# Kernel optimization log

Measured on AMD Instinct MI355X. Metric: run time of the kernel, lower is better.

Reference implementation:

```python
import jax, jax.numpy as jnp
import numpy as np
from jax import lax

B, T, U, H, V = 4, 256, 48, 512, 1024
BLANK = V - 1  # blank = vocab_size - 1, as in Transducer.__init__


def setup_inputs() -> dict:
    key = jax.random.key(0)
    k1, k2, k3, k4 = jax.random.split(key, 4)
    enc_state = jax.random.normal(k1, (B, T, H), jnp.float32)       # encoder output
    dec_state = jax.random.normal(k2, (B, U + 1, H), jnp.float32)   # decoder output (blank-prepended targets)
    W = jax.random.normal(k3, (V, H), jnp.float32) / np.sqrt(H)     # joint proj weight
    b = jnp.zeros((V,), jnp.float32)                                # joint proj bias
    targets = jax.random.randint(k4, (B, U), 0, V - 1).astype(jnp.int32)  # labels, never blank
    inputs_length = jnp.full((B,), T, jnp.int32)
    targets_length = jnp.full((B,), U, jnp.int32)
    return {"enc_state": enc_state, "dec_state": dec_state, "W": W, "b": b,
            "targets": targets, "inputs_length": inputs_length,
            "targets_length": targets_length}


def _rnnt_loss_single(log_probs, targets, t_len, u_len):
    # log_probs: (T, U+1, V); forward-variable alpha DP of RNNT loss.
    lp_blank = log_probs[:, :, BLANK]                                   # (T, U+1)
    lp_label = jnp.take_along_axis(log_probs[:, :-1, :],
                                   targets[None, :, None], axis=2)[..., 0]  # (T, U)
    # first row: only label emissions, alpha[0,u] = sum_{k<u} lp_label[0,k]
    row0 = jnp.concatenate([jnp.zeros((1,), log_probs.dtype),
                            jnp.cumsum(lp_label[0])])                   # (U+1,)

    def row_step(prev_row, t):
        # alpha[t,u] = logaddexp(alpha[t-1,u] + blank[t-1,u], alpha[t,u-1] + label[t,u-1])
        a = prev_row + lp_blank[t - 1]                                  # (U+1,) blank transitions

        def u_step(carry, xs):
            a_u, lab = xs
            cur = jnp.logaddexp(a_u, carry + lab)
            return cur, cur

        _, rest = lax.scan(u_step, a[0], (a[1:], lp_label[t]))
        row = jnp.concatenate([a[:1], rest])
        return row, row

    _, rows = lax.scan(row_step, row0, jnp.arange(1, T))
    alpha = jnp.concatenate([row0[None], rows], axis=0)                 # (T, U+1)
    # negative log-likelihood: final blank emission from (t_len-1, u_len)
    return -(alpha[t_len - 1, u_len] + lp_blank[t_len - 1, u_len])


def reference(enc_state, dec_state, W, b, targets, inputs_length, targets_length):
    # JointNet: broadcast-add (repeat in torch) then linear projection
    joint = enc_state[:, :, None, :] + dec_state[:, None, :, :]         # (B, T, U+1, H)
    logits = jnp.einsum('btuh,vh->btuv', joint, W) + b                  # (B, T, U+1, V)
    log_probs = jax.nn.log_softmax(logits, axis=-1)
    loss = jax.vmap(_rnnt_loss_single)(log_probs, targets, inputs_length, targets_length)
    return loss  # per-sample losses (reduction='None')
```

## Files before the change

### kernel.cpp

```cpp
#include <hip/hip_runtime.h>
#include <math.h>

#define B_ 4
#define T_ 256
#define U_ 48
#define H_ 512
#define V_ 1024
#define BLANK_ (V_-1)

#define GM 1220
#define GM_ENC 1024
#define APAD 1280

#define INVLN2 1.4426950408889634f
#define LN2F   0.6931471805599453f

typedef __attribute__((ext_vector_type(8))) short short8;
typedef __attribute__((ext_vector_type(4))) float f32x4;

__device__ __forceinline__ unsigned short f2bf(float x) {
    union { float f; unsigned int u; } c; c.f = x;
    unsigned int r = c.u + 0x7FFF + ((c.u >> 16) & 1);
    return (unsigned short)(r >> 16);
}
__device__ __forceinline__ float bf2f(unsigned short u) {
    union { unsigned int i; float f; } c; c.i = ((unsigned int)u) << 16; return c.f;
}
__device__ __forceinline__ unsigned int cvt_pk_bf16(float lo, float hi) {
    unsigned int r;
    asm("v_cvt_pk_bf16_f32 %0, %1, %2" : "=v"(r) : "v"(lo), "v"(hi));
    return r;
}
__device__ __forceinline__ int wave_shr1_i(int x, int fill) {
    return __builtin_amdgcn_update_dpp(fill, x, 0x138 , 0xf, 0xf, false);
}
__device__ __forceinline__ float wave_shr1_f(float x, float fill) {
    return __builtin_bit_cast(float,
        wave_shr1_i(__builtin_bit_cast(int, x), __builtin_bit_cast(int, fill)));
}

__global__ __launch_bounds__(256) void gemm1_kernel(
    const float* __restrict__ enc, const float* __restrict__ dec,
    const float* __restrict__ W, const float* __restrict__ bias,
    unsigned short* __restrict__ Pexp)
{
    __shared__ __attribute__((aligned(16))) unsigned short As[64 * 64];
    __shared__ __attribute__((aligned(16))) unsigned short Bs[64 * 64];
    const int tid  = threadIdx.x;
    const int lane = tid & 63, wave = tid >> 6;
    const int wm = wave >> 1, wn = wave & 1;
    const int row0 = blockIdx.y * 64, col0 = blockIdx.x * 64;
    const int srow = tid >> 2;
    const int scg  = (tid & 3) * 16;

    f32x4 acc[2][2];
    #pragma unroll
    for (int mi = 0; mi < 2; ++mi)
        #pragma unroll
        for (int ni = 0; ni < 2; ++ni)
            acc[mi][ni] = (f32x4){0.f, 0.f, 0.f, 0.f};

    const int gr = row0 + srow;
    const float* srcA = (gr < GM_ENC) ? enc + (size_t)gr * H_
                      : (gr < GM)     ? dec + (size_t)(gr - GM_ENC) * H_
                                      : (const float*)0;
    const float* srcB = W + (size_t)(col0 + srow) * H_;

    float4 ra[4], rb[4];
    auto loadAB = [&](int k0) {
        float4 z = make_float4(0.f, 0.f, 0.f, 0.f);
        ra[0] = ra[1] = ra[2] = ra[3] = z;
        if (srcA) {
            const float* s = srcA + k0 + scg;
            ra[0] = *(const float4*)s;       ra[1] = *(const float4*)(s + 4);
            ra[2] = *(const float4*)(s + 8); ra[3] = *(const float4*)(s + 12);
        }
        const float* s = srcB + k0 + scg;
        rb[0] = *(const float4*)s;       rb[1] = *(const float4*)(s + 4);
        rb[2] = *(const float4*)(s + 8); rb[3] = *(const float4*)(s + 12);
    };
    auto stage = [&]() {
        uint4 w0 = { cvt_pk_bf16(ra[0].x, ra[0].y), cvt_pk_bf16(ra[0].z, ra[0].w),
                     cvt_pk_bf16(ra[1].x, ra[1].y), cvt_pk_bf16(ra[1].z, ra[1].w) };
        uint4 w1 = { cvt_pk_bf16(ra[2].x, ra[2].y), cvt_pk_bf16(ra[2].z, ra[2].w),
                     cvt_pk_bf16(ra[3].x, ra[3].y), cvt_pk_bf16(ra[3].z, ra[3].w) };
        uint4 v0 = { cvt_pk_bf16(rb[0].x, rb[0].y), cvt_pk_bf16(rb[0].z, rb[0].w),
                     cvt_pk_bf16(rb[1].x, rb[1].y), cvt_pk_bf16(rb[1].z, rb[1].w) };
        uint4 v1 = { cvt_pk_bf16(rb[2].x, rb[2].y), cvt_pk_bf16(rb[2].z, rb[2].w),
                     cvt_pk_bf16(rb[3].x, rb[3].y), cvt_pk_bf16(rb[3].z, rb[3].w) };
        int colb = scg * 2;
        int sw0 = (colb)      ^ ((srow & 7) << 4);
        int sw1 = (colb + 16) ^ ((srow & 7) << 4);
        *(uint4*)((char*)As + srow * 128 + sw0) = w0;
        *(uint4*)((char*)As + srow * 128 + sw1) = w1;
        *(uint4*)((char*)Bs + srow * 128 + sw0) = v0;
        *(uint4*)((char*)Bs + srow * 128 + sw1) = v1;
    };
    auto compute = [&]() {
        #pragma unroll
        for (int kk = 0; kk < 2; ++kk) {
            short8 a[2], b[2];
            const int cb = kk * 64 + (lane >> 4) * 16;
            #pragma unroll
            for (int mi = 0; mi < 2; ++mi) {
                int r = wm * 32 + mi * 16 + (lane & 15);
                a[mi] = *(const short8*)((const char*)As + r * 128 + (cb ^ ((r & 7) << 4)));
            }
            #pragma unroll
            for (int ni = 0; ni < 2; ++ni) {
                int r = wn * 32 + ni * 16 + (lane & 15);
                b[ni] = *(const short8*)((const char*)Bs + r * 128 + (cb ^ ((r & 7) << 4)));
            }
            #pragma unroll
            for (int mi = 0; mi < 2; ++mi)
                #pragma unroll
                for (int ni = 0; ni < 2; ++ni)
                    asm("v_mfma_f32_16x16x32_bf16 %0, %1, %2, %0"
                        : "+v"(acc[mi][ni]) : "v"(a[mi]), "v"(b[ni]));
        }
    };

    loadAB(0);
    for (int k0 = 0; k0 < H_; k0 += 64) {
        stage();
        asm volatile("s_waitcnt lgkmcnt(0)" ::: "memory");
        __builtin_amdgcn_s_barrier();
        asm volatile("" ::: "memory");
        if (k0 + 64 < H_) loadAB(k0 + 64);
        compute();
        asm volatile("" ::: "memory");
        __builtin_amdgcn_s_barrier();
        asm volatile("" ::: "memory");
    }

    #pragma unroll
    for (int ni = 0; ni < 2; ++ni) {
        int col = col0 + wn * 32 + ni * 16 + (lane & 15);
        float bb = bias[col];
        #pragma unroll
        for (int mi = 0; mi < 2; ++mi) {
            #pragma unroll
            for (int j = 0; j < 4; ++j) {
                int r = row0 + wm * 32 + mi * 16 + (lane >> 4) * 4 + j;
                if (r >= GM) continue;
                float v = acc[mi][ni][j] + (r < GM_ENC ? bb : 0.f);
                Pexp[(size_t)r * V_ + col] = f2bf(__builtin_amdgcn_exp2f(v * INVLN2));
            }
        }
    }
}

__global__ __launch_bounds__(256) void gemm2_kernel(
    const unsigned short* __restrict__ Pexp, const int* __restrict__ targets,
    float* __restrict__ lp)
{
    __shared__ __attribute__((aligned(16))) unsigned short As[64 * 64];
    __shared__ __attribute__((aligned(16))) unsigned short Bs[64 * 64];
    __shared__ float eb[64];
    __shared__ float db[64];
    __shared__ float dg[64];
    __shared__ int   tgts[64];
    const int tid  = threadIdx.x;
    const int lane = tid & 63, wave = tid >> 6;
    const int wm = wave >> 1, wn = wave & 1;
    const int mt = blockIdx.x, b = blockIdx.y;

    if (tid < 64) {
        eb[tid] = bf2f(Pexp[(size_t)(b * 256 + mt * 64 + tid) * V_ + BLANK_]);
    } else if (tid < 128) {
        int u = tid - 64;
        if (u <= U_) {
            size_t drow = (size_t)(GM_ENC + b * (U_ + 1) + u);
            db[u] = bf2f(Pexp[drow * V_ + BLANK_]);
            if (u < U_) {
                int tg = targets[b * U_ + u];
                tgts[u] = tg;
                dg[u] = bf2f(Pexp[drow * V_ + tg]);
            }
        }
    }

    f32x4 acc[2][2];
    #pragma unroll
    for (int mi = 0; mi < 2; ++mi)
        #pragma unroll
        for (int ni = 0; ni < 2; ++ni)
            acc[mi][ni] = (f32x4){0.f, 0.f, 0.f, 0.f};

    short8 a2[2], b2[2];
    auto loadT = [&](int k0) {
        #pragma unroll
        for (int c = 0; c < 2; ++c) {
            int off = (tid + 256 * c) * 16;
            int row = off >> 7, colb = off & 127;
            size_t arow = (size_t)(b * 256 + mt * 64 + row);
            a2[c] = *(const short8*)((const char*)Pexp + arow * (V_*2) + k0*2 + colb);
            size_t brow = (size_t)(GM_ENC + b * (U_ + 1) + (row <= U_ ? row : U_));
            b2[c] = *(const short8*)((const char*)Pexp + brow * (V_*2) + k0*2 + colb);
        }
    };
    auto stageT = [&]() {
        #pragma unroll
        for (int c = 0; c < 2; ++c) {
            int off = (tid + 256 * c) * 16;
            int row = off >> 7, colb = off & 127;
            int sw = colb ^ ((row & 7) << 4);
            *(short8*)((char*)As + row * 128 + sw) = a2[c];
            *(short8*)((char*)Bs + row * 128 + sw) = b2[c];
        }
    };

    loadT(0);
    for (int k0 = 0; k0 < V_; k0 += 64) {
        stageT();
        asm volatile("s_waitcnt lgkmcnt(0)" ::: "memory");
        __builtin_amdgcn_s_barrier();
        asm volatile("" ::: "memory");
        if (k0 + 64 < V_) loadT(k0 + 64);
        #pragma unroll
        for (int kk = 0; kk < 2; ++kk) {
            short8 a[2], bfr[2];
            const int cb = kk * 64 + (lane >> 4) * 16;
            #pragma unroll
            for (int mi = 0; mi < 2; ++mi) {
                int r = wm * 32 + mi * 16 + (lane & 15);
                a[mi] = *(const short8*)((const char*)As + r * 128 + (cb ^ ((r & 7) << 4)));
            }
            #pragma unroll
            for (int ni = 0; ni < 2; ++ni) {
                int r = wn * 32 + ni * 16 + (lane & 15);
                bfr[ni] = *(const short8*)((const char*)Bs + r * 128 + (cb ^ ((r & 7) << 4)));
            }
            #pragma unroll
            for (int mi = 0; mi < 2; ++mi)
                #pragma unroll
                for (int ni = 0; ni < 2; ++ni)
                    asm("v_mfma_f32_16x16x32_bf16 %0, %1, %2, %0"
                        : "+v"(acc[mi][ni]) : "v"(a[mi]), "v"(bfr[ni]));
        }
        asm volatile("" ::: "memory");
        __builtin_amdgcn_s_barrier();
        asm volatile("" ::: "memory");
    }

    #pragma unroll
    for (int ni = 0; ni < 2; ++ni) {
        int u = wn * 32 + ni * 16 + (lane & 15);
        if (u > U_) continue;
        float dbu = db[u];
        float dgu = (u < U_) ? dg[u] : 0.f;
        int   tgu = (u < U_) ? tgts[u] : 0;
        #pragma unroll
        for (int mi = 0; mi < 2; ++mi) {
            #pragma unroll
            for (int j = 0; j < 4; ++j) {
                int tp = wm * 32 + mi * 16 + (lane >> 4) * 4 + j;
                int t  = mt * 64 + tp;
                float rd = __builtin_amdgcn_rcpf(acc[mi][ni][j]);
                lp[((size_t)b * 97 + u) * T_ + t] = eb[tp] * dbu * rd;
                if (u < U_) {
                    float eg = bf2f(Pexp[(size_t)(b * 256 + t) * V_ + tgu]);
                    lp[((size_t)b * 97 + 49 + u) * T_ + t] = eg * dgu * rd;
                }
            }
        }
    }
}

__global__ __launch_bounds__(256) void dp_kernel(
    const float* __restrict__ lp,
    const int* __restrict__ tlen, const int* __restrict__ ulen,
    float* __restrict__ out)
{
    __shared__ __attribute__((aligned(16))) float sm[97 * 257 + 3];
    const int b = blockIdx.x;
    const int tid = threadIdx.x;
    {
        const float4* g = (const float4*)(lp + (size_t)b * 97 * T_);
        for (int i = tid; i < 97 * T_ / 4; i += 256) {
            float4 v = g[i];
            int r = i >> 6;
            int t = (i & 63) << 2;
            float* d = sm + r * 257 + t;
            d[0] = v.x; d[1] = v.y; d[2] = v.z; d[3] = v.w;
        }
    }
    __syncthreads();
    if (tid >= 64) return;

    const int l = tid;
    const int TL = tlen[b], UL = ulen[b];
    const int lt = (TL - 1) >> 2;
    const int smax = lt + UL;

    const int ROWB = 257 * 4;
    const int bLo = 16 * l, bHi = 48 * ROWB + 16 * l;
    const int lLo = 49 * ROWB + 16 * l, lHi = 96 * ROWB + 16 * l;
    int wb = -l * ROWB + 16 * l;

    float M0 = 0.f, M1 = 0.f, M2 = 0.f, M3 = 0.f;
    int E = 0;
    float wprev = 0.f;

    struct Pay { float b0, b1, b2, b3, l0, l1, l2, l3; };
    Pay pA, pB;
    auto issue = [&](Pay& P) {
        int ab = min(max(wb, bLo), bHi);
        int al = min(max(wb + 48 * ROWB, lLo), lHi);
        const char* base = (const char*)sm;
        P.b0 = *(const float*)(base + ab);
        P.b1 = *(const float*)(base + ab + 4);
        P.b2 = *(const float*)(base + ab + 8);
        P.b3 = *(const float*)(base + ab + 12);
        P.l0 = *(const float*)(base + al);
        P.l1 = *(const float*)(base + al + 4);
        P.l2 = *(const float*)(base + al + 8);
        P.l3 = *(const float*)(base + al + 12);
        wb += ROWB;
    };
    auto step = [&](int s, const Pay& P) {
        float bm  = wave_shr1_f(M3, 0.f);
        int   bE  = wave_shr1_i(E, -(1 << 24));
        float B0f = wave_shr1_f(wprev, 0.f);
        wprev = P.b3;
        int u = s - l;
        if (u >= 0 && u <= U_) {
            bool act  = (u == 0);
            bool seed = (s == 0);
            int Eu = act ? bE : max(E, bE);
            if (seed) Eu = 0;
            float sb = ldexpf(bm, bE - Eu);
            float sO = act ? 0.f : ldexpf(1.0f, E - Eu);
            float m0 = M0 * sO, m1 = M1 * sO, m2 = M2 * sO, m3 = M3 * sO;
            float A0 = fmaf(sb, B0f, m0 * P.l0);
            if (seed) A0 = 1.0f;
            float A1 = fmaf(A0, P.b0, m1 * P.l1);
            float A2 = fmaf(A1, P.b1, m2 * P.l2);
            float A3 = fmaf(A2, P.b2, m3 * P.l3);
            float mx = fmaxf(fmaxf(A0, A1), fmaxf(A2, A3));
            int e = (int)((__builtin_bit_cast(unsigned, mx) >> 23) & 0xFF) - 126;
            M0 = ldexpf(A0, -e); M1 = ldexpf(A1, -e);
            M2 = ldexpf(A2, -e); M3 = ldexpf(A3, -e);
            E = Eu + e;
        }
    };

    issue(pA);
    issue(pB);
    int s = 0;
    for (; s + 1 <= smax; s += 2) {
        step(s, pA);     issue(pA);
        step(s + 1, pB); issue(pB);
    }
    if (s <= smax) step(s, pA);

    if (l == lt) {
        int j = (TL - 1) & 3;
        float rm = (j == 0) ? M0 : (j == 1) ? M1 : (j == 2) ? M2 : M3;
        float lfin = __builtin_amdgcn_logf(rm) + (float)E
                   + __builtin_amdgcn_logf(sm[UL * 257 + (TL - 1)]);
        out[b] = -lfin * LN2F;
    }
}

extern "C" void kernel_launch(void* const* d_in, const int* in_sizes, int n_in,
                              void* d_out, int out_size, void* d_ws, size_t ws_size,
                              hipStream_t stream) {
    const float* enc     = (const float*)d_in[0];
    const float* dec     = (const float*)d_in[1];
    const float* W       = (const float*)d_in[2];
    const float* bias    = (const float*)d_in[3];
    const int*   targets = (const int*)d_in[4];
    const int*   tlen    = (const int*)d_in[5];
    const int*   ulen    = (const int*)d_in[6];
    float* out = (float*)d_out;

    unsigned short* Pexp = (unsigned short*)d_ws;
    float* lp = (float*)(Pexp + (size_t)APAD * V_);

    gemm1_kernel<<<dim3(V_/64, APAD/64), dim3(256), 0, stream>>>(
        enc, dec, W, bias, Pexp);

    gemm2_kernel<<<dim3(4, B_), dim3(256), 0, stream>>>(Pexp, targets, lp);

    dp_kernel<<<dim3(B_), dim3(256), 0, stream>>>(lp, tlen, ulen, out);
}
```

Measured before the change: 45.66 us.

## Fuse three kernels into one cooperative kernel with grid syncs

Replaces the three launches (projection GEMM, reduction GEMM, DP) with one cooperative kernel of 256 blocks that runs each stage in turn, separated by grid.sync. The goal is to remove per-launch overhead and the gaps between kernels. In exchange, the first stage now loops 320 tiles over 256 blocks, so some blocks do two tiles, and grid-wide barriers add their own cost. If the cooperative launch fails, the code falls back to the original three kernels.

```diff
diff --git a/kernel.cpp b/kernel.cpp
--- a/kernel.cpp
+++ b/kernel.cpp
@@ -1,5 +1,8 @@
 #include <hip/hip_runtime.h>
+#include <hip/hip_cooperative_groups.h>
 #include <math.h>
+
+namespace cg = cooperative_groups;
 
 #define B_ 4
 #define T_ 256
@@ -37,6 +40,335 @@
 __device__ __forceinline__ float wave_shr1_f(float x, float fill) {
     return __builtin_bit_cast(float,
         wave_shr1_i(__builtin_bit_cast(int, x), __builtin_bit_cast(int, fill)));
+}
+
+__global__ __launch_bounds__(256) void fused_kernel(
+    const float* __restrict__ enc, const float* __restrict__ dec,
+    const float* __restrict__ W, const float* __restrict__ bias,
+    const int* __restrict__ targets, const int* __restrict__ tlen,
+    const int* __restrict__ ulen,
+    unsigned short* __restrict__ Pexp, float* __restrict__ lp,
+    float* __restrict__ out)
+{
+    __shared__ __attribute__((aligned(16))) char smem[(97 * 257 + 3) * 4];
+    __shared__ float eb[64];
+    __shared__ float db[64];
+    __shared__ float dg[64];
+    __shared__ int   tgts[64];
+
+    cg::grid_group grid = cg::this_grid();
+    const int bid  = blockIdx.x;
+    const int tid  = threadIdx.x;
+    const int lane = tid & 63, wave = tid >> 6;
+
+    {
+        unsigned short* As = (unsigned short*)smem;
+        unsigned short* Bs = (unsigned short*)(smem + 8192);
+        const int wm = wave >> 1, wn = wave & 1;
+        const int srow = tid >> 2;
+        const int scg  = (tid & 3) * 16;
+
+        for (int tile = bid; tile < 320; tile += 256) {
+            const int row0 = (tile >> 4) * 64, col0 = (tile & 15) * 64;
+
+            f32x4 acc[2][2];
+            #pragma unroll
+            for (int mi = 0; mi < 2; ++mi)
+                #pragma unroll
+                for (int ni = 0; ni < 2; ++ni)
+                    acc[mi][ni] = (f32x4){0.f, 0.f, 0.f, 0.f};
+
+            const int gr = row0 + srow;
+            const float* srcA = (gr < GM_ENC) ? enc + (size_t)gr * H_
+                              : (gr < GM)     ? dec + (size_t)(gr - GM_ENC) * H_
+                                              : (const float*)0;
+            const float* srcB = W + (size_t)(col0 + srow) * H_;
+
+            float4 ra[4], rb[4];
+            auto loadAB = [&](int k0) {
+                float4 z = make_float4(0.f, 0.f, 0.f, 0.f);
+                ra[0] = ra[1] = ra[2] = ra[3] = z;
+                if (srcA) {
+                    const float* s = srcA + k0 + scg;
+                    ra[0] = *(const float4*)s;       ra[1] = *(const float4*)(s + 4);
+                    ra[2] = *(const float4*)(s + 8); ra[3] = *(const float4*)(s + 12);
+                }
+                const float* s = srcB + k0 + scg;
+                rb[0] = *(const float4*)s;       rb[1] = *(const float4*)(s + 4);
+                rb[2] = *(const float4*)(s + 8); rb[3] = *(const float4*)(s + 12);
+            };
+            auto stage = [&]() {
+                uint4 w0 = { cvt_pk_bf16(ra[0].x, ra[0].y), cvt_pk_bf16(ra[0].z, ra[0].w),
+                             cvt_pk_bf16(ra[1].x, ra[1].y), cvt_pk_bf16(ra[1].z, ra[1].w) };
+                uint4 w1 = { cvt_pk_bf16(ra[2].x, ra[2].y), cvt_pk_bf16(ra[2].z, ra[2].w),
+                             cvt_pk_bf16(ra[3].x, ra[3].y), cvt_pk_bf16(ra[3].z, ra[3].w) };
+                uint4 v0 = { cvt_pk_bf16(rb[0].x, rb[0].y), cvt_pk_bf16(rb[0].z, rb[0].w),
+                             cvt_pk_bf16(rb[1].x, rb[1].y), cvt_pk_bf16(rb[1].z, rb[1].w) };
+                uint4 v1 = { cvt_pk_bf16(rb[2].x, rb[2].y), cvt_pk_bf16(rb[2].z, rb[2].w),
+                             cvt_pk_bf16(rb[3].x, rb[3].y), cvt_pk_bf16(rb[3].z, rb[3].w) };
+                int colb = scg * 2;
+                int sw0 = (colb)      ^ ((srow & 7) << 4);
+                int sw1 = (colb + 16) ^ ((srow & 7) << 4);
+                *(uint4*)((char*)As + srow * 128 + sw0) = w0;
+                *(uint4*)((char*)As + srow * 128 + sw1) = w1;
+                *(uint4*)((char*)Bs + srow * 128 + sw0) = v0;
+                *(uint4*)((char*)Bs + srow * 128 + sw1) = v1;
+            };
+            auto compute = [&]() {
+                #pragma unroll
+                for (int kk = 0; kk < 2; ++kk) {
+                    short8 a[2], b[2];
+                    const int cb = kk * 64 + (lane >> 4) * 16;
+                    #pragma unroll
+                    for (int mi = 0; mi < 2; ++mi) {
+                        int r = wm * 32 + mi * 16 + (lane & 15);
+                        a[mi] = *(const short8*)((const char*)As + r * 128 + (cb ^ ((r & 7) << 4)));
+                    }
+                    #pragma unroll
+                    for (int ni = 0; ni < 2; ++ni) {
+                        int r = wn * 32 + ni * 16 + (lane & 15);
+                        b[ni] = *(const short8*)((const char*)Bs + r * 128 + (cb ^ ((r & 7) << 4)));
+                    }
+                    #pragma unroll
+                    for (int mi = 0; mi < 2; ++mi)
+                        #pragma unroll
+                        for (int ni = 0; ni < 2; ++ni)
+                            asm("v_mfma_f32_16x16x32_bf16 %0, %1, %2, %0"
+                                : "+v"(acc[mi][ni]) : "v"(a[mi]), "v"(b[ni]));
+                }
+            };
+
+            loadAB(0);
+            for (int k0 = 0; k0 < H_; k0 += 64) {
+                stage();
+                asm volatile("s_waitcnt lgkmcnt(0)" ::: "memory");
+                __builtin_amdgcn_s_barrier();
+                asm volatile("" ::: "memory");
+                if (k0 + 64 < H_) loadAB(k0 + 64);
+                compute();
+                asm volatile("" ::: "memory");
+                __builtin_amdgcn_s_barrier();
+                asm volatile("" ::: "memory");
+            }
+
+            #pragma unroll
+            for (int ni = 0; ni < 2; ++ni) {
+                int col = col0 + wn * 32 + ni * 16 + (lane & 15);
+                float bb = bias[col];
+                #pragma unroll
+                for (int mi = 0; mi < 2; ++mi) {
+                    #pragma unroll
+                    for (int j = 0; j < 4; ++j) {
+                        int r = row0 + wm * 32 + mi * 16 + (lane >> 4) * 4 + j;
+                        if (r >= GM) continue;
+                        float v = acc[mi][ni][j] + (r < GM_ENC ? bb : 0.f);
+                        Pexp[(size_t)r * V_ + col] = f2bf(__builtin_amdgcn_exp2f(v * INVLN2));
+                    }
+                }
+            }
+        }
+    }
+    grid.sync();
+
+    if (bid < 16) {
+        unsigned short* As = (unsigned short*)smem;
+        unsigned short* Bs = (unsigned short*)(smem + 8192);
+        const int wm = wave >> 1, wn = wave & 1;
+        const int mt = bid & 3, b = bid >> 2;
+
+        if (tid < 64) {
+            eb[tid] = bf2f(Pexp[(size_t)(b * 256 + mt * 64 + tid) * V_ + BLANK_]);
+        } else if (tid < 128) {
+            int u = tid - 64;
+            if (u <= U_) {
+                size_t drow = (size_t)(GM_ENC + b * (U_ + 1) + u);
+                db[u] = bf2f(Pexp[drow * V_ + BLANK_]);
+                if (u < U_) {
+                    int tg = targets[b * U_ + u];
+                    tgts[u] = tg;
+                    dg[u] = bf2f(Pexp[drow * V_ + tg]);
+                }
+            }
+        }
+
+        f32x4 acc[2][2];
+        #pragma unroll
+        for (int mi = 0; mi < 2; ++mi)
+            #pragma unroll
+            for (int ni = 0; ni < 2; ++ni)
+                acc[mi][ni] = (f32x4){0.f, 0.f, 0.f, 0.f};
+
+        short8 a2[2], b2[2];
+        auto loadT = [&](int k0) {
+            #pragma unroll
+            for (int c = 0; c < 2; ++c) {
+                int off = (tid + 256 * c) * 16;
+                int row = off >> 7, colb = off & 127;
+                size_t arow = (size_t)(b * 256 + mt * 64 + row);
+                a2[c] = *(const short8*)((const char*)Pexp + arow * (V_*2) + k0*2 + colb);
+                size_t brow = (size_t)(GM_ENC + b * (U_ + 1) + (row <= U_ ? row : U_));
+                b2[c] = *(const short8*)((const char*)Pexp + brow * (V_*2) + k0*2 + colb);
+            }
+        };
+        auto stageT = [&]() {
+            #pragma unroll
+            for (int c = 0; c < 2; ++c) {
+                int off = (tid + 256 * c) * 16;
+                int row = off >> 7, colb = off & 127;
+                int sw = colb ^ ((row & 7) << 4);
+                *(short8*)((char*)As + row * 128 + sw) = a2[c];
+                *(short8*)((char*)Bs + row * 128 + sw) = b2[c];
+            }
+        };
+
+        loadT(0);
+        for (int k0 = 0; k0 < V_; k0 += 64) {
+            stageT();
+            asm volatile("s_waitcnt lgkmcnt(0)" ::: "memory");
+            __builtin_amdgcn_s_barrier();
+            asm volatile("" ::: "memory");
+            if (k0 + 64 < V_) loadT(k0 + 64);
+            #pragma unroll
+            for (int kk = 0; kk < 2; ++kk) {
+                short8 a[2], bfr[2];
+                const int cb = kk * 64 + (lane >> 4) * 16;
+                #pragma unroll
+                for (int mi = 0; mi < 2; ++mi) {
+                    int r = wm * 32 + mi * 16 + (lane & 15);
+                    a[mi] = *(const short8*)((const char*)As + r * 128 + (cb ^ ((r & 7) << 4)));
+                }
+                #pragma unroll
+                for (int ni = 0; ni < 2; ++ni) {
+                    int r = wn * 32 + ni * 16 + (lane & 15);
+                    bfr[ni] = *(const short8*)((const char*)Bs + r * 128 + (cb ^ ((r & 7) << 4)));
+                }
+                #pragma unroll
+                for (int mi = 0; mi < 2; ++mi)
+                    #pragma unroll
+                    for (int ni = 0; ni < 2; ++ni)
+                        asm("v_mfma_f32_16x16x32_bf16 %0, %1, %2, %0"
+                            : "+v"(acc[mi][ni]) : "v"(a[mi]), "v"(bfr[ni]));
+            }
+            asm volatile("" ::: "memory");
+            __builtin_amdgcn_s_barrier();
+            asm volatile("" ::: "memory");
+        }
+
+        #pragma unroll
+        for (int ni = 0; ni < 2; ++ni) {
+            int u = wn * 32 + ni * 16 + (lane & 15);
+            if (u > U_) continue;
+            float dbu = db[u];
+            float dgu = (u < U_) ? dg[u] : 0.f;
+            int   tgu = (u < U_) ? tgts[u] : 0;
+            #pragma unroll
+            for (int mi = 0; mi < 2; ++mi) {
+                #pragma unroll
+                for (int j = 0; j < 4; ++j) {
+                    int tp = wm * 32 + mi * 16 + (lane >> 4) * 4 + j;
+                    int t  = mt * 64 + tp;
+                    float rd = __builtin_amdgcn_rcpf(acc[mi][ni][j]);
+                    lp[((size_t)b * 97 + u) * T_ + t] = eb[tp] * dbu * rd;
+                    if (u < U_) {
+                        float eg = bf2f(Pexp[(size_t)(b * 256 + t) * V_ + tgu]);
+                        lp[((size_t)b * 97 + 49 + u) * T_ + t] = eg * dgu * rd;
+                    }
+                }
+            }
+        }
+    }
+    grid.sync();
+
+    if (bid < 4) {
+        const int b = bid;
+        float* sm = (float*)smem;
+        {
+            const float4* g = (const float4*)(lp + (size_t)b * 97 * T_);
+            for (int i = tid; i < 97 * T_ / 4; i += 256) {
+                float4 v = g[i];
+                int r = i >> 6;
+                int t = (i & 63) << 2;
+                float* d = sm + r * 257 + t;
+                d[0] = v.x; d[1] = v.y; d[2] = v.z; d[3] = v.w;
+            }
+        }
+        __syncthreads();
+        if (tid >= 64) return;
+
+        const int l = tid;
+        const int TL = tlen[b], UL = ulen[b];
+        const int lt = (TL - 1) >> 2;
+        const int smax = lt + UL;
+
+        const int ROWB = 257 * 4;
+        const int bLo = 16 * l, bHi = 48 * ROWB + 16 * l;
+        const int lLo = 49 * ROWB + 16 * l, lHi = 96 * ROWB + 16 * l;
+        int wb = -l * ROWB + 16 * l;
+
+        float M0 = 0.f, M1 = 0.f, M2 = 0.f, M3 = 0.f;
+        int E = 0;
+        float wprev = 0.f;
+
+        struct Pay { float b0, b1, b2, b3, l0, l1, l2, l3; };
+        Pay pA, pB;
+        auto issue = [&](Pay& P) {
+            int ab = min(max(wb, bLo), bHi);
+            int al = min(max(wb + 48 * ROWB, lLo), lHi);
+            const char* base = (const char*)sm;
+            P.b0 = *(const float*)(base + ab);
+            P.b1 = *(const float*)(base + ab + 4);
+            P.b2 = *(const float*)(base + ab + 8);
+            P.b3 = *(const float*)(base + ab + 12);
+            P.l0 = *(const float*)(base + al);
+            P.l1 = *(const float*)(base + al + 4);
+            P.l2 = *(const float*)(base + al + 8);
+            P.l3 = *(const float*)(base + al + 12);
+            wb += ROWB;
+        };
+        auto step = [&](int s, const Pay& P) {
+            float bm  = wave_shr1_f(M3, 0.f);
+            int   bE  = wave_shr1_i(E, -(1 << 24));
+            float B0f = wave_shr1_f(wprev, 0.f);
+            wprev = P.b3;
+            int u = s - l;
+            if (u >= 0 && u <= U_) {
+                bool act  = (u == 0);
+                bool seed = (s == 0);
+                int Eu = act ? bE : max(E, bE);
+                if (seed) Eu = 0;
+                float sb = ldexpf(bm, bE - Eu);
+                float sO = act ? 0.f : ldexpf(1.0f, E - Eu);
+                float m0 = M0 * sO, m1 = M1 * sO, m2 = M2 * sO, m3 = M3 * sO;
+                float A0 = fmaf(sb, B0f, m0 * P.l0);
+                if (seed) A0 = 1.0f;
+                float A1 = fmaf(A0, P.b0, m1 * P.l1);
+                float A2 = fmaf(A1, P.b1, m2 * P.l2);
+                float A3 = fmaf(A2, P.b2, m3 * P.l3);
+                float mx = fmaxf(fmaxf(A0, A1), fmaxf(A2, A3));
+                int e = (int)((__builtin_bit_cast(unsigned, mx) >> 23) & 0xFF) - 126;
+                M0 = ldexpf(A0, -e); M1 = ldexpf(A1, -e);
+                M2 = ldexpf(A2, -e); M3 = ldexpf(A3, -e);
+                E = Eu + e;
+            }
+        };
+
+        issue(pA);
+        issue(pB);
+        int s = 0;
+        for (; s + 1 <= smax; s += 2) {
+            step(s, pA);     issue(pA);
+            step(s + 1, pB); issue(pB);
+        }
+        if (s <= smax) step(s, pA);
+
+        if (l == lt) {
+            int j = (TL - 1) & 3;
+            float rm = (j == 0) ? M0 : (j == 1) ? M1 : (j == 2) ? M2 : M3;
+            float lfin = __builtin_amdgcn_logf(rm) + (float)E
+                       + __builtin_amdgcn_logf(sm[UL * 257 + (TL - 1)]);
+            out[b] = -lfin * LN2F;
+        }
+    }
 }
 
 __global__ __launch_bounds__(256) void gemm1_kernel(
@@ -378,10 +710,22 @@
     unsigned short* Pexp = (unsigned short*)d_ws;
     float* lp = (float*)(Pexp + (size_t)APAD * V_);
 
-    gemm1_kernel<<<dim3(V_/64, APAD/64), dim3(256), 0, stream>>>(
-        enc, dec, W, bias, Pexp);
-
-    gemm2_kernel<<<dim3(4, B_), dim3(256), 0, stream>>>(Pexp, targets, lp);
-
-    dp_kernel<<<dim3(B_), dim3(256), 0, stream>>>(lp, tlen, ulen, out);
-}
+    const float *enc_ = enc, *dec_ = dec, *W_ = W, *bias_ = bias;
+    const int *tg_ = targets, *tl_ = tlen, *ul_ = ulen;
+    unsigned short* Pexp_ = Pexp;
+    float* lp_ = lp;
+    float* out_ = out;
+    void* args[] = { (void*)&enc_, (void*)&dec_, (void*)&W_, (void*)&bias_,
+                     (void*)&tg_, (void*)&tl_, (void*)&ul_,
+                     (void*)&Pexp_, (void*)&lp_, (void*)&out_ };
+
+    hipError_t err = hipLaunchCooperativeKernel(
+        (const void*)fused_kernel, dim3(256), dim3(256), args, 0, stream);
+
+    if (err != hipSuccess) {
+        gemm1_kernel<<<dim3(V_/64, APAD/64), dim3(256), 0, stream>>>(
+            enc, dec, W, bias, Pexp);
+        gemm2_kernel<<<dim3(4, B_), dim3(256), 0, stream>>>(Pexp, targets, lp);
+        dp_kernel<<<dim3(B_), dim3(256), 0, stream>>>(lp, tlen, ulen, out);
+    }
+}
```

Result: slower. 122.4 us (+168.1%).
